# Kernel optimization log

Hardware: AMD Instinct MI355X
Metric: run time of the kernel (lower is better)

## Reference

```python
import jax, jax.numpy as jnp
import numpy as np

IN_CH, OUT_CH = 384, 512


def setup_inputs() -> dict:
    key = jax.random.key(0)
    ks = jax.random.split(key, 9)
    B, C, H, W = 8, IN_CH, 48, 48
    s_in = 1.0 / np.sqrt(IN_CH)
    s_out = 1.0 / np.sqrt(OUT_CH)
    return {
        "x": jax.random.normal(ks[0], (B, C, H, W), dtype=jnp.float32),
        "Wq": jax.random.uniform(ks[1], (OUT_CH, IN_CH), jnp.float32, -s_in, s_in),
        "bq": jax.random.uniform(ks[2], (OUT_CH,), jnp.float32, -s_in, s_in),
        "Wk": jax.random.uniform(ks[3], (OUT_CH, IN_CH), jnp.float32, -s_in, s_in),
        "bk": jax.random.uniform(ks[4], (OUT_CH,), jnp.float32, -s_in, s_in),
        "Wv": jax.random.uniform(ks[5], (OUT_CH, IN_CH), jnp.float32, -s_in, s_in),
        "bv": jax.random.uniform(ks[6], (OUT_CH,), jnp.float32, -s_in, s_in),
        "Wo": jax.random.uniform(ks[7], (OUT_CH, OUT_CH), jnp.float32, -s_out, s_out),
        "bo": jax.random.uniform(ks[8], (OUT_CH,), jnp.float32, -s_out, s_out),
    }


def reference(x, Wq, bq, Wk, bk, Wv, bv, Wo, bo):
    B, C, H, W = x.shape
    N = H * W  # number of spatial tokens
    xf = x.reshape(B, C, N)  # [B, C, N]
    # 1x1 convs == per-pixel linear projections
    q = jnp.einsum('oc,bcn->bno', Wq, xf) + bq  # [B, N, O]
    k = jnp.einsum('oc,bcn->bon', Wk, xf) + bk[None, :, None]  # [B, O, N]
    v = jnp.einsum('oc,bcn->bon', Wv, xf) + bv[None, :, None]  # [B, O, N]
    scale = 1.0 / jnp.sqrt(jnp.asarray(Wq.shape[0], x.dtype))
    attn = jax.nn.softmax(jnp.einsum('bno,bom->bnm', q, k) * scale, axis=-1)  # [B, N, N]
    out = jnp.einsum('bom,bnm->bon', v, attn)  # [B, O, N]
    out = jnp.einsum('po,bon->bpn', Wo, out) + bo[None, :, None]
    return out.reshape(B, Wo.shape[0], H, W)
```

## Files before the change

### kernel.cpp

```cpp
#include <hip/hip_runtime.h>
#include <stdint.h>

#define B_    8
#define CIN   384
#define OCH   512
#define NTOK  2304
#define SCALE 0.044194173824159216f

typedef unsigned short u16;
typedef u16   u16x8 __attribute__((ext_vector_type(8)));
typedef short s16x8 __attribute__((ext_vector_type(8)));
typedef float f32x4 __attribute__((ext_vector_type(4)));

__device__ __forceinline__ u16 f2bf(float f) {
    union { uint32_t i; float f; } v; v.f = f;
    uint32_t r = v.i + 0x7fffu + ((v.i >> 16) & 1u);
    return (u16)(r >> 16);
}

typedef __attribute__((address_space(1))) const uint32_t glb_u32;
typedef __attribute__((address_space(3))) uint32_t lds_u32;

__device__ __forceinline__ void gld16(const u16* g, u16* l) {
    __builtin_amdgcn_global_load_lds((glb_u32*)g, (lds_u32*)l, 16, 0, 0);
}

__device__ __forceinline__ size_t baddr(int row, int col, int Kc) {
    return ((size_t)(row >> 4) * (Kc >> 5) + (col >> 5)) * 512
         + (size_t)(((col >> 3) & 3) * 128 + (row & 15) * 8 + (col & 7));
}

__device__ __forceinline__ void stage_blocked(const u16* __restrict__ base,
                                              int row0, int k0, int Kc,
                                              u16* __restrict__ dst, int t)
{
    const int lane = t & 63;
    const int w = t >> 6;
    const int bpr = Kc >> 5;
#pragma unroll
    for (int it = 0; it < 2; ++it) {
        const int ck = w * 2 + it;
        const u16* gp = base + ((size_t)((row0 >> 4) + ck) * bpr + (k0 >> 5)) * 512
                      + (size_t)lane * 8;
        u16* lp = dst + ck * 512;
        __builtin_amdgcn_global_load_lds((glb_u32*)gp, (lds_u32*)lp, 16, 0, 0);
    }
}

__device__ __forceinline__ void mfma_core(const u16* __restrict__ As,
                                          const u16* __restrict__ Bs,
                                          int wm16, int wn16, int lrow, int kq,
                                          f32x4 acc[4][4])
{
    s16x8 a[4], b[4];
#pragma unroll
    for (int i = 0; i < 4; ++i)
        a[i] = *(const s16x8*)(As + (((wm16 + i) * 64) + kq * 16 + lrow) * 8);
#pragma unroll
    for (int j = 0; j < 4; ++j)
        b[j] = *(const s16x8*)(Bs + (((wn16 + j) * 64) + kq * 16 + lrow) * 8);
#pragma unroll
    for (int i = 0; i < 4; ++i)
#pragma unroll
        for (int j = 0; j < 4; ++j)
            acc[i][j] = __builtin_amdgcn_mfma_f32_16x16x32_bf16(a[i], b[j], acc[i][j], 0, 0, 0);
}

template <int MODE, int K>
__device__ __forceinline__ void gemm64_core(
    u16* __restrict__ sm,
    const u16* __restrict__ A, const u16* __restrict__ Bp,
    const float* __restrict__ aux, void* __restrict__ Cout,
    int N, int m0, int n0)
{
    constexpr int NT = K / 32;
    u16* As0 = sm;
    u16* Bs0 = sm + 2048;
    u16* As1 = sm + 4096;
    u16* Bs1 = sm + 6144;

    const int ln = threadIdx.x & 63;
    const int lrow = ln & 15, kq = ln >> 4;

    const int bpr = K >> 5;
    const size_t rstep = (size_t)bpr << 9;
    const u16* pA = A  + (((size_t)(m0 >> 4) * bpr) << 9) + (size_t)(ln << 3);
    const u16* pB = Bp + (((size_t)(n0 >> 4) * bpr) << 9) + (size_t)(ln << 3);

    f32x4 acc[4][4] = {};

#define STAGE8(ga, gb, Ad, Bd)                                             \
    gld16((ga),             (Ad));        gld16((ga) + rstep,     (Ad) + 512);  \
    gld16((ga) + 2 * rstep, (Ad) + 1024); gld16((ga) + 3 * rstep, (Ad) + 1536); \
    gld16((gb),             (Bd));        gld16((gb) + rstep,     (Bd) + 512);  \
    gld16((gb) + 2 * rstep, (Bd) + 1024); gld16((gb) + 3 * rstep, (Bd) + 1536);

    STAGE8(pA, pB, As0, Bs0)

#pragma unroll 1
    for (int kt = 0; kt < NT; kt += 2) {
        STAGE8(pA + 512, pB + 512, As1, Bs1)
        asm volatile("s_waitcnt vmcnt(8)" ::: "memory");
        mfma_core(As0, Bs0, 0, 0, lrow, kq, acc);
        asm volatile("" ::: "memory");
        if (kt + 2 < NT) {
            STAGE8(pA + 1024, pB + 1024, As0, Bs0)
            asm volatile("s_waitcnt vmcnt(8)" ::: "memory");
        } else {
            asm volatile("s_waitcnt vmcnt(0)" ::: "memory");
        }
        mfma_core(As1, Bs1, 0, 0, lrow, kq, acc);
        asm volatile("" ::: "memory");
        pA += 1024; pB += 1024;
    }
#undef STAGE8

    const int offl = ((lrow >> 3) << 7) + (lrow & 7) + (kq << 5);

    if constexpr (MODE == 1) {
        u16* C = (u16*)Cout;
        float bcol[4];
#pragma unroll
        for (int j = 0; j < 4; ++j) bcol[j] = aux[n0 + j * 16 + lrow];
#pragma unroll
        for (int i = 0; i < 4; ++i) {
            u16* Crow = C + ((size_t)((m0 >> 4) + i) * (N >> 5) + (n0 >> 5)) * 512 + offl;
#pragma unroll
            for (int j = 0; j < 4; ++j) {
                u16* Cj = Crow + (j >> 1) * 512 + ((j & 1) << 8);
#pragma unroll
                for (int r = 0; r < 4; ++r)
                    Cj[r * 8] = f2bf(acc[i][j][r] + bcol[j]);
            }
        }
    } else if constexpr (MODE == 2) {
        u16* C = (u16*)Cout;
#pragma unroll
        for (int i = 0; i < 4; ++i) {
            const float4 b4 = *(const float4*)(aux + m0 + i * 16 + kq * 4);
            u16* Crow = C + ((size_t)((m0 >> 4) + i) * (N >> 5) + (n0 >> 5)) * 512 + offl;
#pragma unroll
            for (int j = 0; j < 4; ++j) {
                u16* Cj = Crow + (j >> 1) * 512 + ((j & 1) << 8);
                Cj[0]  = f2bf(acc[i][j][0] + b4.x);
                Cj[8]  = f2bf(acc[i][j][1] + b4.y);
                Cj[16] = f2bf(acc[i][j][2] + b4.z);
                Cj[24] = f2bf(acc[i][j][3] + b4.w);
            }
        }
    } else if constexpr (MODE == 3) {
        u16* C = (u16*)Cout;
#pragma unroll
        for (int i = 0; i < 4; ++i) {
            const float4 rs4 = *(const float4*)(aux + m0 + i * 16 + kq * 4);
            const float inv0 = 1.0f / rs4.x, inv1 = 1.0f / rs4.y;
            const float inv2 = 1.0f / rs4.z, inv3 = 1.0f / rs4.w;
            u16* Crow = C + ((size_t)((m0 >> 4) + i) * (N >> 5) + (n0 >> 5)) * 512 + offl;
#pragma unroll
            for (int j = 0; j < 4; ++j) {
                u16* Cj = Crow + (j >> 1) * 512 + ((j & 1) << 8);
                Cj[0]  = f2bf(acc[i][j][0] * inv0);
                Cj[8]  = f2bf(acc[i][j][1] * inv1);
                Cj[16] = f2bf(acc[i][j][2] * inv2);
                Cj[24] = f2bf(acc[i][j][3] * inv3);
            }
        }
    } else {
        float* C = (float*)Cout;
#pragma unroll
        for (int i = 0; i < 4; ++i) {
            const int row = m0 + i * 16 + kq * 4;
            const float4 b4 = *(const float4*)(aux + row);
            const float bv4[4] = {b4.x, b4.y, b4.z, b4.w};
#pragma unroll
            for (int r = 0; r < 4; ++r)
#pragma unroll
                for (int j = 0; j < 4; ++j)
                    C[(size_t)(row + r) * N + n0 + j * 16 + lrow] = acc[i][j][r] + bv4[r];
        }
    }
}

#define WQKV_SZ (OCH * CIN)
#define WO_SZ   (OCH * OCH)
#define CH_QKV  (WQKV_SZ / 8)
#define CH_WO   (WO_SZ / 8)
#define CH_TOT  (3 * CH_QKV + CH_WO)

__global__ __launch_bounds__(256) void prep_w_kernel(
    const float* __restrict__ Wq, const float* __restrict__ Wk,
    const float* __restrict__ Wv, const float* __restrict__ Wo,
    u16* __restrict__ Wqb, u16* __restrict__ Wkb,
    u16* __restrict__ Wvb, u16* __restrict__ Wob)
{
    int lc = blockIdx.x * 256 + threadIdx.x;
    if (lc >= CH_TOT) return;
    const float* src; u16* dst; int Kc;
    if      (lc < CH_QKV)     { src = Wq; dst = Wqb; Kc = CIN; }
    else if (lc < 2 * CH_QKV) { src = Wk; dst = Wkb; Kc = CIN; lc -= CH_QKV; }
    else if (lc < 3 * CH_QKV) { src = Wv; dst = Wvb; Kc = CIN; lc -= 2 * CH_QKV; }
    else                      { src = Wo; dst = Wob; Kc = OCH; lc -= 3 * CH_QKV; }
    const int brick = lc >> 6, l = lc & 63;
    const int bpr = Kc >> 5;
    const int g = brick / bpr, c = brick % bpr;
    const int row = g * 16 + (l & 15);
    const int col = c * 32 + (l >> 4) * 8;
    const float* s = src + (size_t)row * Kc + col;
    float4 v0 = *(const float4*)s;
    float4 v1 = *(const float4*)(s + 4);
    u16x8 o;
    o[0] = f2bf(v0.x); o[1] = f2bf(v0.y); o[2] = f2bf(v0.z); o[3] = f2bf(v0.w);
    o[4] = f2bf(v1.x); o[5] = f2bf(v1.y); o[6] = f2bf(v1.z); o[7] = f2bf(v1.w);
    *(u16x8*)(dst + (size_t)lc * 8) = o;
}

__global__ __launch_bounds__(256) void transpose_x_kernel(
    const float* __restrict__ x, u16* __restrict__ xT)
{
    const int n0 = blockIdx.x * 64;
    const int c0 = blockIdx.y * 64;
    const int b  = blockIdx.z;
    const float* X = x + (size_t)b * CIN * NTOK;

    __shared__ float Ts[64][66];

    const int t = threadIdx.x;
#pragma unroll
    for (int rep = 0; rep < 4; ++rep) {
        const int cr = (t >> 4) + rep * 16;
        const int n4 = (t & 15) * 4;
        float4 v = *(const float4*)(X + (size_t)(c0 + cr) * NTOK + n0 + n4);
        *(float2*)&Ts[cr][n4]     = make_float2(v.x, v.y);
        *(float2*)&Ts[cr][n4 + 2] = make_float2(v.z, v.w);
    }
    __syncthreads();

    u16* O = xT + (size_t)b * NTOK * CIN;
#pragma unroll
    for (int rep = 0; rep < 2; ++rep) {
        const int nr = (t >> 3) + rep * 32;
        const int c8 = (t & 7) * 8;
        u16 tmp[8];
#pragma unroll
        for (int j = 0; j < 8; ++j) tmp[j] = f2bf(Ts[c8 + j][nr]);
        *(u16x8*)(O + baddr(n0 + nr, c0 + c8, CIN)) = *(const u16x8*)tmp;
    }
}

__global__ __launch_bounds__(64) void qkv64_kernel(
    const u16* __restrict__ xT,
    const u16* __restrict__ Wqb, const float* __restrict__ bq,
    const u16* __restrict__ Wkb, const float* __restrict__ bk,
    const u16* __restrict__ Wvb, const float* __restrict__ bv,
    u16* __restrict__ Qt, u16* __restrict__ Kt, u16* __restrict__ Vw)
{
    __shared__ __align__(16) u16 sm[8192];
    const int sel = blockIdx.x % 24;
    const int b = sel & 7, which = sel >> 3;
    const int rem = blockIdx.x / 24;
    const u16* xTb = xT + (size_t)b * NTOK * CIN;
    if (which < 2) {
        const int n0 = (rem & 7) * 64, m0 = (rem >> 3) * 64;
        gemm64_core<1, CIN>(sm, xTb, which ? Wkb : Wqb, which ? bk : bq,
            (which ? Kt : Qt) + (size_t)b * NTOK * OCH, OCH, m0, n0);
    } else {
        const int n0 = (rem % 36) * 64, m0 = (rem / 36) * 64;
        gemm64_core<2, CIN>(sm, Wvb, xTb, bv,
            Vw + (size_t)b * OCH * NTOK, NTOK, m0, n0);
    }
}

__global__ __launch_bounds__(256) void logits_exp_kernel(
    const u16* __restrict__ Qt, const u16* __restrict__ Kt,
    u16* __restrict__ Ew, float* __restrict__ rowsumG)
{
    const int z   = blockIdx.x % B_;
    const int rem = blockIdx.x / B_;
    const int n0 = (rem % (NTOK / 128)) * 128;
    const int m0 = (rem / (NTOK / 128)) * 128;
    const u16* A  = Qt + (size_t)z * NTOK * OCH;
    const u16* Bp = Kt + (size_t)z * NTOK * OCH;

    __shared__ u16 As[128 * 32];
    __shared__ u16 Bs[128 * 32];
    __shared__ float rowsumL[128];

    const int t = threadIdx.x;
    const int w = t >> 6, ln = t & 63;
    const int wm16 = (w & 1) * 4, wn16 = (w >> 1) * 4;
    const int lrow = ln & 15, kq = ln >> 4;

    if (t < 128) rowsumL[t] = 0.f;

    f32x4 acc[4][4] = {};

    for (int k0 = 0; k0 < OCH; k0 += 32) {
        stage_blocked(A, m0, k0, OCH, As, t);
        stage_blocked(Bp, n0, k0, OCH, Bs, t);
        __syncthreads();
        mfma_core(As, Bs, wm16, wn16, lrow, kq, acc);
        __syncthreads();
    }

    u16* E = Ew + (size_t)z * NTOK * NTOK;
    const int offl = ((lrow >> 3) << 7) + (lrow & 7) + (kq << 5);
#pragma unroll
    for (int i = 0; i < 4; ++i) {
        u16* Erow = E + ((size_t)((m0 >> 4) + wm16 + i) * (NTOK >> 5) + (n0 >> 5)) * 512 + offl;
#pragma unroll
        for (int r = 0; r < 4; ++r) {
            float part = 0.f;
#pragma unroll
            for (int j = 0; j < 4; ++j) {
                float e = __expf(acc[i][j][r] * SCALE);
                part += e;
                Erow[((wn16 + j) >> 1) * 512 + ((j & 1) << 8) + r * 8] = f2bf(e);
            }
            part += __shfl_xor(part, 1);
            part += __shfl_xor(part, 2);
            part += __shfl_xor(part, 4);
            part += __shfl_xor(part, 8);
            if (lrow == 0) atomicAdd(&rowsumL[(wm16 + i) * 16 + kq * 4 + r], part);
        }
    }
    __syncthreads();
    if (t < 128) atomicAdd(&rowsumG[(size_t)z * NTOK + m0 + t], rowsumL[t]);
}

__global__ __launch_bounds__(64) void pv64_kernel(
    const u16* __restrict__ Ew, const u16* __restrict__ Vw,
    const float* __restrict__ rowsumG, u16* __restrict__ AOt)
{
    __shared__ __align__(16) u16 sm[8192];
    const int z = blockIdx.x & 7;
    const int rem = blockIdx.x >> 3;
    const int n0 = (rem & 7) * 64, m0 = (rem >> 3) * 64;
    gemm64_core<3, NTOK>(sm, Ew + (size_t)z * NTOK * NTOK, Vw + (size_t)z * OCH * NTOK,
        rowsumG + (size_t)z * NTOK, AOt + (size_t)z * NTOK * OCH, OCH, m0, n0);
}

__global__ __launch_bounds__(64) void out64_kernel(
    const u16* __restrict__ Wob, const u16* __restrict__ AOt,
    const float* __restrict__ bo, float* __restrict__ out)
{
    __shared__ __align__(16) u16 sm[8192];
    const int z = blockIdx.x & 7;
    const int rem = blockIdx.x >> 3;
    const int n0 = (rem % 36) * 64, m0 = (rem / 36) * 64;
    gemm64_core<4, OCH>(sm, Wob, AOt + (size_t)z * NTOK * OCH, bo,
        out + (size_t)z * OCH * NTOK, NTOK, m0, n0);
}

extern "C" void kernel_launch(void* const* d_in, const int* in_sizes, int n_in,
                              void* d_out, int out_size, void* d_ws, size_t ws_size,
                              hipStream_t stream)
{
    const float* x  = (const float*)d_in[0];
    const float* Wq = (const float*)d_in[1];
    const float* bq = (const float*)d_in[2];
    const float* Wk = (const float*)d_in[3];
    const float* bk = (const float*)d_in[4];
    const float* Wv = (const float*)d_in[5];
    const float* bv = (const float*)d_in[6];
    const float* Wo = (const float*)d_in[7];
    const float* bo = (const float*)d_in[8];
    float* out = (float*)d_out;

    u16* ws = (u16*)d_ws;
    u16* Wqb = ws;
    u16* Wkb = Wqb + WQKV_SZ;
    u16* Wvb = Wkb + WQKV_SZ;
    u16* Wob = Wvb + WQKV_SZ;
    u16* xT  = Wob + WO_SZ;
    const size_t xtsz  = (size_t)B_ * NTOK * CIN;
    const size_t qkvsz = (size_t)B_ * NTOK * OCH;
    u16* Qt  = xT + xtsz;
    u16* Kt  = Qt + qkvsz;
    u16* Vw  = Kt + qkvsz;
    u16* Ew  = Vw + qkvsz;
    float* rowsumG = (float*)(Ew + (size_t)B_ * NTOK * NTOK);
    u16* AOt = Qt;

    dim3 blk(256), blk64(64);

    prep_w_kernel<<<dim3((CH_TOT + 255) / 256), blk, 0, stream>>>(
        Wq, Wk, Wv, Wo, Wqb, Wkb, Wvb, Wob);
    transpose_x_kernel<<<dim3(NTOK / 64, CIN / 64, B_), blk, 0, stream>>>(x, xT);
    hipMemsetAsync(rowsumG, 0, (size_t)B_ * NTOK * sizeof(float), stream);

    qkv64_kernel<<<dim3(288 * 24), blk64, 0, stream>>>(
        xT, Wqb, bq, Wkb, bk, Wvb, bv, Qt, Kt, Vw);

    logits_exp_kernel<<<dim3(18 * 18 * B_), blk, 0, stream>>>(Qt, Kt, Ew, rowsumG);

    pv64_kernel<<<dim3(288 * 8), blk64, 0, stream>>>(Ew, Vw, rowsumG, AOt);

    out64_kernel<<<dim3(288 * 8), blk64, 0, stream>>>(Wob, AOt, bo, out);
}
```

Baseline: 286.7 us.

## Merge weight prep and x transpose launches; retile PV GEMM to 128x128 blocks

Combines the weight bf16 conversion and the x transpose into one kernel launch, selecting the role by block index, which removes one launch. Replaces the 64-thread, 64x64-tile PV kernel with a 256-thread, 128x128-tile kernel built on the shared stage_blocked/mfma_core helpers, with the rowsum division in its epilogue. Larger tiles improve operand reuse for the large E·V product, but the grid shrinks from 2304 to 576 blocks, which may lower occupancy and latency hiding over the long K loop, which has no double buffering.

```diff
diff --git a/kernel.cpp b/kernel.cpp
--- a/kernel.cpp
+++ b/kernel.cpp
@@ -148,23 +148,6 @@
                 Cj[24] = f2bf(acc[i][j][3] + b4.w);
             }
         }
-    } else if constexpr (MODE == 3) {
-        u16* C = (u16*)Cout;
-#pragma unroll
-        for (int i = 0; i < 4; ++i) {
-            const float4 rs4 = *(const float4*)(aux + m0 + i * 16 + kq * 4);
-            const float inv0 = 1.0f / rs4.x, inv1 = 1.0f / rs4.y;
-            const float inv2 = 1.0f / rs4.z, inv3 = 1.0f / rs4.w;
-            u16* Crow = C + ((size_t)((m0 >> 4) + i) * (N >> 5) + (n0 >> 5)) * 512 + offl;
-#pragma unroll
-            for (int j = 0; j < 4; ++j) {
-                u16* Cj = Crow + (j >> 1) * 512 + ((j & 1) << 8);
-                Cj[0]  = f2bf(acc[i][j][0] * inv0);
-                Cj[8]  = f2bf(acc[i][j][1] * inv1);
-                Cj[16] = f2bf(acc[i][j][2] * inv2);
-                Cj[24] = f2bf(acc[i][j][3] * inv3);
-            }
-        }
     } else {
         float* C = (float*)Cout;
 #pragma unroll
@@ -186,45 +169,47 @@
 #define CH_QKV  (WQKV_SZ / 8)
 #define CH_WO   (WO_SZ / 8)
 #define CH_TOT  (3 * CH_QKV + CH_WO)
-
-__global__ __launch_bounds__(256) void prep_w_kernel(
+#define PREP_BLK (CH_TOT / 256)
+#define TRX_BLK  ((NTOK / 64) * (CIN / 64) * B_)
+
+__global__ __launch_bounds__(256) void prep_kernel(
     const float* __restrict__ Wq, const float* __restrict__ Wk,
     const float* __restrict__ Wv, const float* __restrict__ Wo,
     u16* __restrict__ Wqb, u16* __restrict__ Wkb,
-    u16* __restrict__ Wvb, u16* __restrict__ Wob)
-{
-    int lc = blockIdx.x * 256 + threadIdx.x;
-    if (lc >= CH_TOT) return;
-    const float* src; u16* dst; int Kc;
-    if      (lc < CH_QKV)     { src = Wq; dst = Wqb; Kc = CIN; }
-    else if (lc < 2 * CH_QKV) { src = Wk; dst = Wkb; Kc = CIN; lc -= CH_QKV; }
-    else if (lc < 3 * CH_QKV) { src = Wv; dst = Wvb; Kc = CIN; lc -= 2 * CH_QKV; }
-    else                      { src = Wo; dst = Wob; Kc = OCH; lc -= 3 * CH_QKV; }
-    const int brick = lc >> 6, l = lc & 63;
-    const int bpr = Kc >> 5;
-    const int g = brick / bpr, c = brick % bpr;
-    const int row = g * 16 + (l & 15);
-    const int col = c * 32 + (l >> 4) * 8;
-    const float* s = src + (size_t)row * Kc + col;
-    float4 v0 = *(const float4*)s;
-    float4 v1 = *(const float4*)(s + 4);
-    u16x8 o;
-    o[0] = f2bf(v0.x); o[1] = f2bf(v0.y); o[2] = f2bf(v0.z); o[3] = f2bf(v0.w);
-    o[4] = f2bf(v1.x); o[5] = f2bf(v1.y); o[6] = f2bf(v1.z); o[7] = f2bf(v1.w);
-    *(u16x8*)(dst + (size_t)lc * 8) = o;
-}
-
-__global__ __launch_bounds__(256) void transpose_x_kernel(
+    u16* __restrict__ Wvb, u16* __restrict__ Wob,
     const float* __restrict__ x, u16* __restrict__ xT)
 {
-    const int n0 = blockIdx.x * 64;
-    const int c0 = blockIdx.y * 64;
-    const int b  = blockIdx.z;
+    __shared__ float Ts[64][66];
+    const int t = threadIdx.x;
+
+    if (blockIdx.x < PREP_BLK) {
+        int lc = blockIdx.x * 256 + t;
+        const float* src; u16* dst; int Kc;
+        if      (lc < CH_QKV)     { src = Wq; dst = Wqb; Kc = CIN; }
+        else if (lc < 2 * CH_QKV) { src = Wk; dst = Wkb; Kc = CIN; lc -= CH_QKV; }
+        else if (lc < 3 * CH_QKV) { src = Wv; dst = Wvb; Kc = CIN; lc -= 2 * CH_QKV; }
+        else                      { src = Wo; dst = Wob; Kc = OCH; lc -= 3 * CH_QKV; }
+        const int brick = lc >> 6, l = lc & 63;
+        const int bpr = Kc >> 5;
+        const int g = brick / bpr, c = brick % bpr;
+        const int row = g * 16 + (l & 15);
+        const int col = c * 32 + (l >> 4) * 8;
+        const float* s = src + (size_t)row * Kc + col;
+        float4 v0 = *(const float4*)s;
+        float4 v1 = *(const float4*)(s + 4);
+        u16x8 o;
+        o[0] = f2bf(v0.x); o[1] = f2bf(v0.y); o[2] = f2bf(v0.z); o[3] = f2bf(v0.w);
+        o[4] = f2bf(v1.x); o[5] = f2bf(v1.y); o[6] = f2bf(v1.z); o[7] = f2bf(v1.w);
+        *(u16x8*)(dst + (size_t)lc * 8) = o;
+        return;
+    }
+
+    const int tb = blockIdx.x - PREP_BLK;
+    const int n0 = (tb % 36) * 64;
+    const int c0 = ((tb / 36) % 6) * 64;
+    const int b  = tb / 216;
     const float* X = x + (size_t)b * CIN * NTOK;
 
-    __shared__ float Ts[64][66];
-
-    const int t = threadIdx.x;
 #pragma unroll
     for (int rep = 0; rep < 4; ++rep) {
         const int cr = (t >> 4) + rep * 16;
@@ -327,16 +312,52 @@
     if (t < 128) atomicAdd(&rowsumG[(size_t)z * NTOK + m0 + t], rowsumL[t]);
 }
 
-__global__ __launch_bounds__(64) void pv64_kernel(
+__global__ __launch_bounds__(256) void pv_div_kernel(
     const u16* __restrict__ Ew, const u16* __restrict__ Vw,
     const float* __restrict__ rowsumG, u16* __restrict__ AOt)
 {
-    __shared__ __align__(16) u16 sm[8192];
-    const int z = blockIdx.x & 7;
-    const int rem = blockIdx.x >> 3;
-    const int n0 = (rem & 7) * 64, m0 = (rem >> 3) * 64;
-    gemm64_core<3, NTOK>(sm, Ew + (size_t)z * NTOK * NTOK, Vw + (size_t)z * OCH * NTOK,
-        rowsumG + (size_t)z * NTOK, AOt + (size_t)z * NTOK * OCH, OCH, m0, n0);
+    const int z   = blockIdx.x % B_;
+    const int rem = blockIdx.x / B_;
+    const int n0 = (rem % 4) * 128;
+    const int m0 = (rem / 4) * 128;
+    const u16* A  = Ew + (size_t)z * NTOK * NTOK;
+    const u16* Bp = Vw + (size_t)z * OCH * NTOK;
+
+    __shared__ u16 As[128 * 32];
+    __shared__ u16 Bs[128 * 32];
+
+    const int t = threadIdx.x;
+    const int w = t >> 6, ln = t & 63;
+    const int wm16 = (w & 1) * 4, wn16 = (w >> 1) * 4;
+    const int lrow = ln & 15, kq = ln >> 4;
+
+    f32x4 acc[4][4] = {};
+
+    for (int k0 = 0; k0 < NTOK; k0 += 32) {
+        stage_blocked(A, m0, k0, NTOK, As, t);
+        stage_blocked(Bp, n0, k0, NTOK, Bs, t);
+        __syncthreads();
+        mfma_core(As, Bs, wm16, wn16, lrow, kq, acc);
+        __syncthreads();
+    }
+
+    u16* AO = AOt + (size_t)z * NTOK * OCH;
+    const int offl = ((lrow >> 3) << 7) + (lrow & 7) + (kq << 5);
+#pragma unroll
+    for (int i = 0; i < 4; ++i) {
+        const float4 rs4 = *(const float4*)(rowsumG + (size_t)z * NTOK + m0 + (wm16 + i) * 16 + kq * 4);
+        const float inv0 = 1.0f / rs4.x, inv1 = 1.0f / rs4.y;
+        const float inv2 = 1.0f / rs4.z, inv3 = 1.0f / rs4.w;
+        u16* Crow = AO + ((size_t)((m0 >> 4) + wm16 + i) * (OCH >> 5) + (n0 >> 5)) * 512 + offl;
+#pragma unroll
+        for (int j = 0; j < 4; ++j) {
+            u16* Cj = Crow + ((wn16 + j) >> 1) * 512 + ((j & 1) << 8);
+            Cj[0]  = f2bf(acc[i][j][0] * inv0);
+            Cj[8]  = f2bf(acc[i][j][1] * inv1);
+            Cj[16] = f2bf(acc[i][j][2] * inv2);
+            Cj[24] = f2bf(acc[i][j][3] * inv3);
+        }
+    }
 }
 
 __global__ __launch_bounds__(64) void out64_kernel(
@@ -383,17 +404,17 @@
 
     dim3 blk(256), blk64(64);
 
-    prep_w_kernel<<<dim3((CH_TOT + 255) / 256), blk, 0, stream>>>(
-        Wq, Wk, Wv, Wo, Wqb, Wkb, Wvb, Wob);
-    transpose_x_kernel<<<dim3(NTOK / 64, CIN / 64, B_), blk, 0, stream>>>(x, xT);
     hipMemsetAsync(rowsumG, 0, (size_t)B_ * NTOK * sizeof(float), stream);
+
+    prep_kernel<<<dim3(PREP_BLK + TRX_BLK), blk, 0, stream>>>(
+        Wq, Wk, Wv, Wo, Wqb, Wkb, Wvb, Wob, x, xT);
 
     qkv64_kernel<<<dim3(288 * 24), blk64, 0, stream>>>(
         xT, Wqb, bq, Wkb, bk, Wvb, bv, Qt, Kt, Vw);
 
     logits_exp_kernel<<<dim3(18 * 18 * B_), blk, 0, stream>>>(Qt, Kt, Ew, rowsumG);
 
-    pv64_kernel<<<dim3(288 * 8), blk64, 0, stream>>>(Ew, Vw, rowsumG, AOt);
+    pv_div_kernel<<<dim3(4 * 18 * B_), blk, 0, stream>>>(Ew, Vw, rowsumG, AOt);
 
     out64_kernel<<<dim3(288 * 8), blk64, 0, stream>>>(Wob, AOt, bo, out);
 }
```

New measurement: 270.2 us. 1.06x faster.
